# Kernel optimization log

Hardware: AMD Instinct MI355X
Metric: run time of the kernel (lower is better)

## Reference

```python
import jax, jax.numpy as jnp
import numpy as np

B, S, D = 4, 2048, 256


def setup_inputs() -> dict:
    key = jax.random.key(0)
    ks = jax.random.split(key, 8)
    context = jax.random.normal(ks[0], (B, S, D), dtype=jnp.float32)
    eos_mask = jax.random.randint(ks[1], (B, S, S), 0, 2, dtype=jnp.int32)
    prior = jax.random.uniform(ks[2], (B, S, S), dtype=jnp.float32)
    Wq = jax.random.normal(ks[3], (D, D), dtype=jnp.float32) * 0.02
    bq = jnp.zeros((D,), dtype=jnp.float32)
    Wk = jax.random.normal(ks[4], (D, D), dtype=jnp.float32) * 0.02
    bk = jnp.zeros((D,), dtype=jnp.float32)
    ln_a = jnp.ones((D,), dtype=jnp.float32)
    ln_b = jnp.zeros((D,), dtype=jnp.float32)
    return {"context": context, "prior": prior, "Wq": Wq, "bq": bq,
            "Wk": Wk, "bk": bk, "ln_a": ln_a, "ln_b": ln_b,
            "eos_mask": eos_mask}


def reference(context, prior, Wq, bq, Wk, bk, ln_a, ln_b, eos_mask):
    seq = context.shape[1]
    # LayerNorm (torch: unbiased std, eps added to std)
    mean = context.mean(axis=-1, keepdims=True)
    std = jnp.std(context, axis=-1, ddof=1, keepdims=True)
    x = ln_a * (context - mean) / (std + 1e-6) + ln_b

    idx = jnp.arange(seq)
    diff = idx[None, :] - idx[:, None]
    a = diff == 1                      # superdiagonal
    offdiag = jnp.abs(diff) == 1       # a + c (super + sub diagonal)
    eye = diff == 0                    # b
    tri = jnp.triu(jnp.ones((seq, seq), dtype=jnp.float32))

    # mask = eos_mask & (a + c)  (precedence: & binds looser than +)
    mask = jnp.bitwise_and(eos_mask, offdiag.astype(jnp.int32))

    # torch Linear: y = x @ W.T + b
    query = x @ Wq.T + bq
    key = x @ Wk.T + bk
    scores = jnp.einsum('bqd,bkd->bqk', query, key) / 256.0
    scores = jnp.where(mask == 0, -1e9, scores)
    neibor = jax.nn.softmax(scores, axis=-1)
    neibor = jnp.sqrt(neibor * neibor.transpose(0, 2, 1) + 1e-9)
    neibor = prior + (1.0 - prior) * neibor

    # log -> zero except superdiagonal -> triangular matmul -> exp
    t = jnp.where(a, jnp.log(neibor + 1e-9), 0.0) @ tri   # [B,S,S]
    g = jnp.exp(jnp.matmul(tri, t))                        # [B,S,S]
    strict_upper = jnp.logical_and(tri.astype(bool), jnp.logical_not(eye))
    g = jnp.where(strict_upper, g, 0.0)  # masked_fill(tri - b == 0, 0)
    g = g + g.transpose(0, 2, 1) + jnp.where(eye, neibor, 1e-9)
    return g
```

## Files before the change

### kernel.cpp

```cpp
#include <hip/hip_runtime.h>
#include <math.h>

#define SS 2048
#define DD 256
#define NB 4
#define NR (NB * SS)

__global__ __launch_bounds__(256) void prep_kernel(
    const float* __restrict__ Wq, const float* __restrict__ Wk,
    const float* __restrict__ bq, float* __restrict__ A, float* __restrict__ u) {
    int t = threadIdx.x;
    int d = blockIdx.x;
    if (d < DD) {
        float a0 = 0.f, a1 = 0.f, a2 = 0.f, a3 = 0.f;
        for (int i = 0; i < DD; i += 4) {
            a0 += Wq[(i + 0) * DD + d] * Wk[(i + 0) * DD + t];
            a1 += Wq[(i + 1) * DD + d] * Wk[(i + 1) * DD + t];
            a2 += Wq[(i + 2) * DD + d] * Wk[(i + 2) * DD + t];
            a3 += Wq[(i + 3) * DD + d] * Wk[(i + 3) * DD + t];
        }
        A[d * DD + t] = (a0 + a1) + (a2 + a3);
    } else {
        float a0 = 0.f, a1 = 0.f, a2 = 0.f, a3 = 0.f;
        for (int i = 0; i < DD; i += 4) {
            a0 += Wk[(i + 0) * DD + t] * bq[i + 0];
            a1 += Wk[(i + 1) * DD + t] * bq[i + 1];
            a2 += Wk[(i + 2) * DD + t] * bq[i + 2];
            a3 += Wk[(i + 3) * DD + t] * bq[i + 3];
        }
        u[t] = (a0 + a1) + (a2 + a3);
    }
}

#define XP 260
#define FMA4(accv, a, bv) \
    accv.x += (a) * bv.x; accv.y += (a) * bv.y; \
    accv.z += (a) * bv.z; accv.w += (a) * bv.w;

__global__ __launch_bounds__(256) void gemm_score_kernel(
    const float4* __restrict__ ctx4, const float4* __restrict__ ln_a4,
    const float4* __restrict__ ln_b4, const float* __restrict__ A,
    const float* __restrict__ u, const int* __restrict__ eos,
    float4* __restrict__ pvals) {
    __shared__ float Xn[34][XP];
    int tid = threadIdx.x;
    int lane = tid & 63;
    int wave = tid >> 6;
    int row0 = blockIdx.x * 32;
    const float4* A4 = (const float4*)A;

    float4 ga = ln_a4[lane], gb = ln_b4[lane];
    for (int rr = wave; rr < 34; rr += 4) {
        int g = row0 - 1 + rr;
        g = (g < 0) ? 0 : (g > NR - 1 ? NR - 1 : g);
        float4 v = ctx4[(size_t)g * 64 + lane];
        float s = v.x + v.y + v.z + v.w;
#pragma unroll
        for (int off = 32; off > 0; off >>= 1) s += __shfl_xor(s, off, 64);
        float mean = s * (1.0f / 256.0f);
        float4 dd = make_float4(v.x - mean, v.y - mean, v.z - mean, v.w - mean);
        float s2 = dd.x * dd.x + dd.y * dd.y + dd.z * dd.z + dd.w * dd.w;
#pragma unroll
        for (int off = 32; off > 0; off >>= 1) s2 += __shfl_xor(s2, off, 64);
        float inv = 1.0f / (sqrtf(s2 * (1.0f / 255.0f)) + 1e-6f);
        float* xr = &Xn[rr][lane * 4];
        xr[0] = ga.x * dd.x * inv + gb.x;
        xr[1] = ga.y * dd.y * inv + gb.y;
        xr[2] = ga.z * dd.z * inv + gb.z;
        xr[3] = ga.w * dd.w * inv + gb.w;
    }
    __syncthreads();

    int tx = tid & 15, ty = tid >> 4;
    float4 acc[2][4] = {};
    const float* xr0 = &Xn[1 + ty * 2][0];
    const float* xr1 = &Xn[2 + ty * 2][0];
#pragma unroll 4
    for (int k = 0; k < DD; k++) {
        float a0 = xr0[k];
        float a1 = xr1[k];
        float4 b0 = A4[(size_t)k * 64 + tx];
        float4 b1 = A4[(size_t)k * 64 + tx + 16];
        float4 b2 = A4[(size_t)k * 64 + tx + 32];
        float4 b3 = A4[(size_t)k * 64 + tx + 48];
        FMA4(acc[0][0], a0, b0) FMA4(acc[0][1], a0, b1)
        FMA4(acc[0][2], a0, b2) FMA4(acc[0][3], a0, b3)
        FMA4(acc[1][0], a1, b0) FMA4(acc[1][1], a1, b1)
        FMA4(acc[1][2], a1, b2) FMA4(acc[1][3], a1, b3)
    }

    const float4* u4 = (const float4*)u;
#pragma unroll
    for (int q = 0; q < 4; q++) {
        float4 uv = u4[q * 16 + tx];
        acc[0][q].x += uv.x; acc[0][q].y += uv.y; acc[0][q].z += uv.z; acc[0][q].w += uv.w;
        acc[1][q].x += uv.x; acc[1][q].y += uv.y; acc[1][q].z += uv.z; acc[1][q].w += uv.w;
    }
#pragma unroll
    for (int i = 0; i < 2; i++) {
        int li = 1 + ty * 2 + i;
        int r = row0 + ty * 2 + i;
        int s = r & (SS - 1), b = r >> 11;
        bool has_n = (s < SS - 1), has_p = (s > 0);
        float fn = has_n ? 1.0f : 0.0f, fp = has_p ? 1.0f : 0.0f;
        float partial = 0.0f;
#pragma unroll
        for (int q = 0; q < 4; q++) {
            int c = q * 64 + tx * 4;
            float wx = fn * Xn[li + 1][c + 0] - fp * Xn[li - 1][c + 0];
            float wy = fn * Xn[li + 1][c + 1] - fp * Xn[li - 1][c + 1];
            float wz = fn * Xn[li + 1][c + 2] - fp * Xn[li - 1][c + 2];
            float ww = fn * Xn[li + 1][c + 3] - fp * Xn[li - 1][c + 3];
            partial += acc[i][q].x * wx + acc[i][q].y * wy
                     + acc[i][q].z * wz + acc[i][q].w * ww;
        }
#pragma unroll
        for (int off = 8; off > 0; off >>= 1) partial += __shfl_xor(partial, off, 64);
        if (tx == 0) {
            size_t base = (size_t)b * SS * SS + (size_t)s * SS;
            bool mn = has_n && (eos[base + s + 1] != 0);
            bool mp = has_p && (eos[base + s - 1] != 0);
            float pn, pp, pd;
            if (mn && mp) {
                float d = partial * (1.0f / 256.0f);
                pn = 1.0f / (1.0f + __expf(-d));
                pp = 1.0f - pn;
                pd = 0.0f;
            } else if (mn) { pn = 1.0f; pp = 0.0f; pd = 0.0f; }
            else if (mp)   { pn = 0.0f; pp = 1.0f; pd = 0.0f; }
            else           { pn = pp = pd = (1.0f / 2048.0f); }
            pvals[r] = make_float4(pn, pp, pd, 0.0f);
        }
    }
}

__global__ __launch_bounds__(256) void scan_kernel(
    const float4* __restrict__ pvals, const float* __restrict__ prior,
    float* __restrict__ P) {
    int b = blockIdx.x, t = threadIdx.x;
    int base_s = t * 8;
    double loc[8];
    double run = 0.0;
#pragma unroll
    for (int i = 0; i < 8; i++) {
        loc[i] = run;
        int s = base_s + i;
        float lv = 0.0f;
        if (s < SS - 1) {
            int r = b * SS + s;
            float4 pv = pvals[r];
            float4 pv1 = pvals[r + 1];
            float ns = sqrtf(pv.x * pv1.y + 1e-9f);
            float pr = prior[(size_t)b * SS * SS + (size_t)s * SS + s + 1];
            float neib = pr + (1.0f - pr) * ns;
            lv = logf(neib + 1e-9f);
        }
        run += (double)lv;
    }
    int lane = t & 63, wave = t >> 6;
    double v = run;
#pragma unroll
    for (int off = 1; off < 64; off <<= 1) {
        double uu = __shfl_up(v, off, 64);
        if (lane >= off) v += uu;
    }
    __shared__ double wsum[4];
    if (lane == 63) wsum[wave] = v;
    __syncthreads();
    double woff = 0.0;
    for (int w = 0; w < wave; w++) woff += wsum[w];
    double texcl = woff + (v - run);
#pragma unroll
    for (int i = 0; i < 8; i++)
        P[b * SS + base_s + i] = (float)(texcl + loc[i]);
}

__global__ __launch_bounds__(256) void fill_kernel(
    const float* __restrict__ P, const float4* __restrict__ pvals,
    const float* __restrict__ prior, float* __restrict__ out) {
    int blk = blockIdx.x;
    int i = blk & (SS - 1), b = blk >> 11;
    int t = threadIdx.x;
    __shared__ float shPi, shDv;
    if (t == 0) {
        shPi = P[blk];
        float pd = pvals[blk].z;
        float prd = prior[(size_t)b * SS * SS + (size_t)i * SS + i];
        shDv = prd + (1.0f - prd) * sqrtf(pd * pd + 1e-9f);
    }
    __syncthreads();
    float Pi = shPi, dv = shDv;
    const float* Pb = P + b * SS;
    size_t outbase = (size_t)blk * SS;
    float4 pj0 = *(const float4*)(Pb + t * 8);
    float4 pj1 = *(const float4*)(Pb + t * 8 + 4);
    float pj[8] = {pj0.x, pj0.y, pj0.z, pj0.w, pj1.x, pj1.y, pj1.z, pj1.w};
    float res[8];
#pragma unroll
    for (int k = 0; k < 8; k++) {
        int j = t * 8 + k;
        float d = (j > i) ? (pj[k] - Pi) : (Pi - pj[k]);
        float val = __expf(d) + 1e-9f;
        res[k] = (j == i) ? dv : val;
    }
    *(float4*)(out + outbase + t * 8) = make_float4(res[0], res[1], res[2], res[3]);
    *(float4*)(out + outbase + t * 8 + 4) = make_float4(res[4], res[5], res[6], res[7]);
}

extern "C" void kernel_launch(void* const* d_in, const int* in_sizes, int n_in,
                              void* d_out, int out_size, void* d_ws, size_t ws_size,
                              hipStream_t stream) {
    const float* context = (const float*)d_in[0];
    const float* prior   = (const float*)d_in[1];
    const float* Wq      = (const float*)d_in[2];
    const float* bq      = (const float*)d_in[3];
    const float* Wk      = (const float*)d_in[4];
    const float* ln_a    = (const float*)d_in[6];
    const float* ln_b    = (const float*)d_in[7];
    const int*   eos     = (const int*)d_in[8];
    float* out = (float*)d_out;

    float* ws = (float*)d_ws;
    float* A     = ws;
    float* u     = ws + 65536;
    float4* pv   = (float4*)(ws + 65792);
    float* P     = ws + 98560;

    prep_kernel<<<DD + 1, 256, 0, stream>>>(Wq, Wk, bq, A, u);
    gemm_score_kernel<<<NR / 32, 256, 0, stream>>>(
        (const float4*)context, (const float4*)ln_a, (const float4*)ln_b,
        A, u, eos, pv);
    scan_kernel<<<NB, 256, 0, stream>>>(pv, prior, P);
    fill_kernel<<<NR, 256, 0, stream>>>(P, pv, prior, out);
}
```

Before: 250.4 us.

## Stage A tiles in LDS and use a transposed X tile in the score GEMM

The score GEMM is restructured. Each block now stages 32x256 chunks of A in shared memory and keeps a transposed copy of the normalized rows, so each thread computes a 4-row by 8-column tile with float4 LDS reads instead of streaming A from global memory per thread. Partial dot products are reduced across waves through a small shared buffer. This raises LDS use to roughly 104 KB per block, which lowers occupancy and adds barriers, to cut global traffic on A. The whole output still comes from the fill kernel, which likely dominates the run time.

```diff
diff --git a/kernel.cpp b/kernel.cpp
--- a/kernel.cpp
+++ b/kernel.cpp
@@ -33,6 +33,7 @@
 }
 
 #define XP 260
+#define XTP 36
 #define FMA4(accv, a, bv) \
     accv.x += (a) * bv.x; accv.y += (a) * bv.y; \
     accv.z += (a) * bv.z; accv.w += (a) * bv.w;
@@ -43,6 +44,9 @@
     const float* __restrict__ u, const int* __restrict__ eos,
     float4* __restrict__ pvals) {
     __shared__ float Xn[34][XP];
+    __shared__ float XnT[256][XTP];
+    __shared__ float As[32][256];
+    __shared__ float red[32][4];
     int tid = threadIdx.x;
     int lane = tid & 63;
     int wave = tid >> 6;
@@ -71,66 +75,99 @@
     }
     __syncthreads();
 
-    int tx = tid & 15, ty = tid >> 4;
-    float4 acc[2][4] = {};
-    const float* xr0 = &Xn[1 + ty * 2][0];
-    const float* xr1 = &Xn[2 + ty * 2][0];
-#pragma unroll 4
-    for (int k = 0; k < DD; k++) {
-        float a0 = xr0[k];
-        float a1 = xr1[k];
-        float4 b0 = A4[(size_t)k * 64 + tx];
-        float4 b1 = A4[(size_t)k * 64 + tx + 16];
-        float4 b2 = A4[(size_t)k * 64 + tx + 32];
-        float4 b3 = A4[(size_t)k * 64 + tx + 48];
-        FMA4(acc[0][0], a0, b0) FMA4(acc[0][1], a0, b1)
-        FMA4(acc[0][2], a0, b2) FMA4(acc[0][3], a0, b3)
-        FMA4(acc[1][0], a1, b0) FMA4(acc[1][1], a1, b1)
-        FMA4(acc[1][2], a1, b2) FMA4(acc[1][3], a1, b3)
+    {
+        int r = tid >> 3;
+        int kq = (tid & 7) * 32;
+        const float* src = &Xn[1 + r][kq];
+#pragma unroll
+        for (int j = 0; j < 32; j++) XnT[kq + j][r] = src[j];
+    }
+
+    int lx = lane & 7;
+    int ly = lane >> 3;
+    float4 acc[4][2] = {};
+    const float4* As4 = (const float4*)As;
+    int bidx = wave * 16 + lx * 2;
+    for (int k0 = 0; k0 < DD; k0 += 32) {
+#pragma unroll
+        for (int q = 0; q < 8; q++) {
+            int f4 = q * 256 + tid;
+            int k = f4 >> 6, c4 = f4 & 63;
+            *(float4*)&As[k][c4 * 4] = A4[(size_t)(k0 + k) * 64 + c4];
+        }
+        __syncthreads();
+        const float4* pX = (const float4*)&XnT[k0][0] + ly;
+        const float4* pB = As4 + bidx;
+#pragma unroll 8
+        for (int k = 0; k < 32; k++) {
+            float4 a4 = pX[k * 9];
+            float4 b0 = pB[k * 64];
+            float4 b1 = pB[k * 64 + 1];
+            FMA4(acc[0][0], a4.x, b0) FMA4(acc[0][1], a4.x, b1)
+            FMA4(acc[1][0], a4.y, b0) FMA4(acc[1][1], a4.y, b1)
+            FMA4(acc[2][0], a4.z, b0) FMA4(acc[2][1], a4.z, b1)
+            FMA4(acc[3][0], a4.w, b0) FMA4(acc[3][1], a4.w, b1)
+        }
+        __syncthreads();
     }
 
     const float4* u4 = (const float4*)u;
-#pragma unroll
-    for (int q = 0; q < 4; q++) {
-        float4 uv = u4[q * 16 + tx];
-        acc[0][q].x += uv.x; acc[0][q].y += uv.y; acc[0][q].z += uv.z; acc[0][q].w += uv.w;
-        acc[1][q].x += uv.x; acc[1][q].y += uv.y; acc[1][q].z += uv.z; acc[1][q].w += uv.w;
-    }
-#pragma unroll
-    for (int i = 0; i < 2; i++) {
-        int li = 1 + ty * 2 + i;
-        int r = row0 + ty * 2 + i;
+    {
+        float4 uv0 = u4[bidx], uv1 = u4[bidx + 1];
+#pragma unroll
+        for (int i = 0; i < 4; i++) {
+            acc[i][0].x += uv0.x; acc[i][0].y += uv0.y;
+            acc[i][0].z += uv0.z; acc[i][0].w += uv0.w;
+            acc[i][1].x += uv1.x; acc[i][1].y += uv1.y;
+            acc[i][1].z += uv1.z; acc[i][1].w += uv1.w;
+        }
+    }
+    int c = wave * 64 + lx * 8;
+#pragma unroll
+    for (int i = 0; i < 4; i++) {
+        int row = ly * 4 + i;
+        int li = 1 + row;
+        int r = row0 + row;
+        int s = r & (SS - 1);
+        bool has_n = (s < SS - 1), has_p = (s > 0);
+        float fn = has_n ? 1.0f : 0.0f, fp = has_p ? 1.0f : 0.0f;
+        float4 n0 = *(const float4*)&Xn[li + 1][c];
+        float4 n1 = *(const float4*)&Xn[li + 1][c + 4];
+        float4 p0 = *(const float4*)&Xn[li - 1][c];
+        float4 p1 = *(const float4*)&Xn[li - 1][c + 4];
+        float partial =
+            acc[i][0].x * (fn * n0.x - fp * p0.x) +
+            acc[i][0].y * (fn * n0.y - fp * p0.y) +
+            acc[i][0].z * (fn * n0.z - fp * p0.z) +
+            acc[i][0].w * (fn * n0.w - fp * p0.w) +
+            acc[i][1].x * (fn * n1.x - fp * p1.x) +
+            acc[i][1].y * (fn * n1.y - fp * p1.y) +
+            acc[i][1].z * (fn * n1.z - fp * p1.z) +
+            acc[i][1].w * (fn * n1.w - fp * p1.w);
+#pragma unroll
+        for (int off = 4; off > 0; off >>= 1) partial += __shfl_xor(partial, off, 64);
+        if (lx == 0) red[row][wave] = partial;
+    }
+    __syncthreads();
+    if (tid < 32) {
+        int row = tid;
+        int r = row0 + row;
         int s = r & (SS - 1), b = r >> 11;
         bool has_n = (s < SS - 1), has_p = (s > 0);
-        float fn = has_n ? 1.0f : 0.0f, fp = has_p ? 1.0f : 0.0f;
-        float partial = 0.0f;
-#pragma unroll
-        for (int q = 0; q < 4; q++) {
-            int c = q * 64 + tx * 4;
-            float wx = fn * Xn[li + 1][c + 0] - fp * Xn[li - 1][c + 0];
-            float wy = fn * Xn[li + 1][c + 1] - fp * Xn[li - 1][c + 1];
-            float wz = fn * Xn[li + 1][c + 2] - fp * Xn[li - 1][c + 2];
-            float ww = fn * Xn[li + 1][c + 3] - fp * Xn[li - 1][c + 3];
-            partial += acc[i][q].x * wx + acc[i][q].y * wy
-                     + acc[i][q].z * wz + acc[i][q].w * ww;
-        }
-#pragma unroll
-        for (int off = 8; off > 0; off >>= 1) partial += __shfl_xor(partial, off, 64);
-        if (tx == 0) {
-            size_t base = (size_t)b * SS * SS + (size_t)s * SS;
-            bool mn = has_n && (eos[base + s + 1] != 0);
-            bool mp = has_p && (eos[base + s - 1] != 0);
-            float pn, pp, pd;
-            if (mn && mp) {
-                float d = partial * (1.0f / 256.0f);
-                pn = 1.0f / (1.0f + __expf(-d));
-                pp = 1.0f - pn;
-                pd = 0.0f;
-            } else if (mn) { pn = 1.0f; pp = 0.0f; pd = 0.0f; }
-            else if (mp)   { pn = 0.0f; pp = 1.0f; pd = 0.0f; }
-            else           { pn = pp = pd = (1.0f / 2048.0f); }
-            pvals[r] = make_float4(pn, pp, pd, 0.0f);
-        }
+        float partial = (red[row][0] + red[row][1]) + (red[row][2] + red[row][3]);
+        size_t base = (size_t)b * SS * SS + (size_t)s * SS;
+        bool mn = has_n && (eos[base + s + 1] != 0);
+        bool mp = has_p && (eos[base + s - 1] != 0);
+        float pn, pp, pd;
+        if (mn && mp) {
+            float d = partial * (1.0f / 256.0f);
+            pn = 1.0f / (1.0f + __expf(-d));
+            pp = 1.0f - pn;
+            pd = 0.0f;
+        } else if (mn) { pn = 1.0f; pp = 0.0f; pd = 0.0f; }
+        else if (mp)   { pn = 0.0f; pp = 1.0f; pd = 0.0f; }
+        else           { pn = pp = pd = (1.0f / 2048.0f); }
+        pvals[r] = make_float4(pn, pp, pd, 0.0f);
     }
 }
 
```

New measurement: 227.7 us. 9.0% less time.

## Stage projection matrix tiles in LDS and give each wave eight rows

Applied to the files above, without the earlier changes.

The score GEMM now loads 64-row tiles of the combined Wq^T·Wk matrix into shared memory. Each wave computes eight normalized rows against all 256 output columns, reusing every LDS value across eight rows. This replaces the per-thread global reads of A, which were repeated for every row pair. The cost is a large LDS footprint (about 99KB per block), extra barriers, and a different reduction that collects per-row dot products by wave-wide shuffles.

```diff
diff --git a/kernel.cpp b/kernel.cpp
--- a/kernel.cpp
+++ b/kernel.cpp
@@ -33,6 +33,7 @@
 }
 
 #define XP 260
+#define BK 64
 #define FMA4(accv, a, bv) \
     accv.x += (a) * bv.x; accv.y += (a) * bv.y; \
     accv.z += (a) * bv.z; accv.w += (a) * bv.w;
@@ -43,6 +44,7 @@
     const float* __restrict__ u, const int* __restrict__ eos,
     float4* __restrict__ pvals) {
     __shared__ float Xn[34][XP];
+    __shared__ float As[BK][256];
     int tid = threadIdx.x;
     int lane = tid & 63;
     int wave = tid >> 6;
@@ -63,74 +65,101 @@
 #pragma unroll
         for (int off = 32; off > 0; off >>= 1) s2 += __shfl_xor(s2, off, 64);
         float inv = 1.0f / (sqrtf(s2 * (1.0f / 255.0f)) + 1e-6f);
-        float* xr = &Xn[rr][lane * 4];
-        xr[0] = ga.x * dd.x * inv + gb.x;
-        xr[1] = ga.y * dd.y * inv + gb.y;
-        xr[2] = ga.z * dd.z * inv + gb.z;
-        xr[3] = ga.w * dd.w * inv + gb.w;
-    }
-    __syncthreads();
-
-    int tx = tid & 15, ty = tid >> 4;
-    float4 acc[2][4] = {};
-    const float* xr0 = &Xn[1 + ty * 2][0];
-    const float* xr1 = &Xn[2 + ty * 2][0];
+        float4 xv;
+        xv.x = ga.x * dd.x * inv + gb.x;
+        xv.y = ga.y * dd.y * inv + gb.y;
+        xv.z = ga.z * dd.z * inv + gb.z;
+        xv.w = ga.w * dd.w * inv + gb.w;
+        *(float4*)&Xn[rr][lane * 4] = xv;
+    }
+
+    float4 acc[8] = {};
+    const float4* As4 = (const float4*)As;
+    int rbase = 1 + wave * 8;
+    for (int k0 = 0; k0 < DD; k0 += BK) {
+        __syncthreads();
+#pragma unroll
+        for (int q = 0; q < (BK * 64) / 256; q++) {
+            int f4 = q * 256 + tid;
+            int k = f4 >> 6, c4 = f4 & 63;
+            *(float4*)&As[k][c4 * 4] = A4[(size_t)(k0 + k) * 64 + c4];
+        }
+        __syncthreads();
 #pragma unroll 4
-    for (int k = 0; k < DD; k++) {
-        float a0 = xr0[k];
-        float a1 = xr1[k];
-        float4 b0 = A4[(size_t)k * 64 + tx];
-        float4 b1 = A4[(size_t)k * 64 + tx + 16];
-        float4 b2 = A4[(size_t)k * 64 + tx + 32];
-        float4 b3 = A4[(size_t)k * 64 + tx + 48];
-        FMA4(acc[0][0], a0, b0) FMA4(acc[0][1], a0, b1)
-        FMA4(acc[0][2], a0, b2) FMA4(acc[0][3], a0, b3)
-        FMA4(acc[1][0], a1, b0) FMA4(acc[1][1], a1, b1)
-        FMA4(acc[1][2], a1, b2) FMA4(acc[1][3], a1, b3)
-    }
-
-    const float4* u4 = (const float4*)u;
-#pragma unroll
-    for (int q = 0; q < 4; q++) {
-        float4 uv = u4[q * 16 + tx];
-        acc[0][q].x += uv.x; acc[0][q].y += uv.y; acc[0][q].z += uv.z; acc[0][q].w += uv.w;
-        acc[1][q].x += uv.x; acc[1][q].y += uv.y; acc[1][q].z += uv.z; acc[1][q].w += uv.w;
-    }
-#pragma unroll
-    for (int i = 0; i < 2; i++) {
-        int li = 1 + ty * 2 + i;
-        int r = row0 + ty * 2 + i;
+        for (int kk = 0; kk < BK; kk += 4) {
+            float4 av[8];
+#pragma unroll
+            for (int i = 0; i < 8; i++)
+                av[i] = *(const float4*)&Xn[rbase + i][k0 + kk];
+            float4 b;
+            b = As4[(size_t)(kk + 0) * 64 + lane];
+            FMA4(acc[0], av[0].x, b) FMA4(acc[1], av[1].x, b)
+            FMA4(acc[2], av[2].x, b) FMA4(acc[3], av[3].x, b)
+            FMA4(acc[4], av[4].x, b) FMA4(acc[5], av[5].x, b)
+            FMA4(acc[6], av[6].x, b) FMA4(acc[7], av[7].x, b)
+            b = As4[(size_t)(kk + 1) * 64 + lane];
+            FMA4(acc[0], av[0].y, b) FMA4(acc[1], av[1].y, b)
+            FMA4(acc[2], av[2].y, b) FMA4(acc[3], av[3].y, b)
+            FMA4(acc[4], av[4].y, b) FMA4(acc[5], av[5].y, b)
+            FMA4(acc[6], av[6].y, b) FMA4(acc[7], av[7].y, b)
+            b = As4[(size_t)(kk + 2) * 64 + lane];
+            FMA4(acc[0], av[0].z, b) FMA4(acc[1], av[1].z, b)
+            FMA4(acc[2], av[2].z, b) FMA4(acc[3], av[3].z, b)
+            FMA4(acc[4], av[4].z, b) FMA4(acc[5], av[5].z, b)
+            FMA4(acc[6], av[6].z, b) FMA4(acc[7], av[7].z, b)
+            b = As4[(size_t)(kk + 3) * 64 + lane];
+            FMA4(acc[0], av[0].w, b) FMA4(acc[1], av[1].w, b)
+            FMA4(acc[2], av[2].w, b) FMA4(acc[3], av[3].w, b)
+            FMA4(acc[4], av[4].w, b) FMA4(acc[5], av[5].w, b)
+            FMA4(acc[6], av[6].w, b) FMA4(acc[7], av[7].w, b)
+        }
+    }
+
+    {
+        float4 uv = ((const float4*)u)[lane];
+#pragma unroll
+        for (int i = 0; i < 8; i++) {
+            acc[i].x += uv.x; acc[i].y += uv.y;
+            acc[i].z += uv.z; acc[i].w += uv.w;
+        }
+    }
+    float myp = 0.0f;
+#pragma unroll
+    for (int i = 0; i < 8; i++) {
+        int li = rbase + i;
+        int r = row0 + wave * 8 + i;
+        int s = r & (SS - 1);
+        float fn = (s < SS - 1) ? 1.0f : 0.0f;
+        float fp = (s > 0) ? 1.0f : 0.0f;
+        float4 n1 = *(const float4*)&Xn[li + 1][lane * 4];
+        float4 p1 = *(const float4*)&Xn[li - 1][lane * 4];
+        float partial =
+            acc[i].x * (fn * n1.x - fp * p1.x) +
+            acc[i].y * (fn * n1.y - fp * p1.y) +
+            acc[i].z * (fn * n1.z - fp * p1.z) +
+            acc[i].w * (fn * n1.w - fp * p1.w);
+#pragma unroll
+        for (int off = 32; off > 0; off >>= 1)
+            partial += __shfl_xor(partial, off, 64);
+        myp = (lane == i) ? partial : myp;
+    }
+    if (lane < 8) {
+        int r = row0 + wave * 8 + lane;
         int s = r & (SS - 1), b = r >> 11;
         bool has_n = (s < SS - 1), has_p = (s > 0);
-        float fn = has_n ? 1.0f : 0.0f, fp = has_p ? 1.0f : 0.0f;
-        float partial = 0.0f;
-#pragma unroll
-        for (int q = 0; q < 4; q++) {
-            int c = q * 64 + tx * 4;
-            float wx = fn * Xn[li + 1][c + 0] - fp * Xn[li - 1][c + 0];
-            float wy = fn * Xn[li + 1][c + 1] - fp * Xn[li - 1][c + 1];
-            float wz = fn * Xn[li + 1][c + 2] - fp * Xn[li - 1][c + 2];
-            float ww = fn * Xn[li + 1][c + 3] - fp * Xn[li - 1][c + 3];
-            partial += acc[i][q].x * wx + acc[i][q].y * wy
-                     + acc[i][q].z * wz + acc[i][q].w * ww;
-        }
-#pragma unroll
-        for (int off = 8; off > 0; off >>= 1) partial += __shfl_xor(partial, off, 64);
-        if (tx == 0) {
-            size_t base = (size_t)b * SS * SS + (size_t)s * SS;
-            bool mn = has_n && (eos[base + s + 1] != 0);
-            bool mp = has_p && (eos[base + s - 1] != 0);
-            float pn, pp, pd;
-            if (mn && mp) {
-                float d = partial * (1.0f / 256.0f);
-                pn = 1.0f / (1.0f + __expf(-d));
-                pp = 1.0f - pn;
-                pd = 0.0f;
-            } else if (mn) { pn = 1.0f; pp = 0.0f; pd = 0.0f; }
-            else if (mp)   { pn = 0.0f; pp = 1.0f; pd = 0.0f; }
-            else           { pn = pp = pd = (1.0f / 2048.0f); }
-            pvals[r] = make_float4(pn, pp, pd, 0.0f);
-        }
+        size_t base = (size_t)b * SS * SS + (size_t)s * SS;
+        bool mn = has_n && (eos[base + s + 1] != 0);
+        bool mp = has_p && (eos[base + s - 1] != 0);
+        float pn, pp, pd;
+        if (mn && mp) {
+            float d = myp * (1.0f / 256.0f);
+            pn = 1.0f / (1.0f + __expf(-d));
+            pp = 1.0f - pn;
+            pd = 0.0f;
+        } else if (mn) { pn = 1.0f; pp = 0.0f; pd = 0.0f; }
+        else if (mp)   { pn = 0.0f; pp = 1.0f; pd = 0.0f; }
+        else           { pn = pp = pd = (1.0f / 2048.0f); }
+        pvals[r] = make_float4(pn, pp, pd, 0.0f);
     }
 }
 
```

Measured after the change: 225.4 us. -10.0%, faster.

## Stage A matrix tiles in shared memory with register double-buffering

Applied to the files above, without the earlier changes.

The GEMM loop in the score kernel now copies 64-row chunks of the 256x256 A matrix into LDS cooperatively, instead of having every thread read A straight from global memory each k step. The inner loop is software-pipelined: the LDS operands for step k+2 are loaded while the FMAs for step k run. This targets global/L2 load latency in a loop bound by memory reads. In exchange it adds 64 KB of LDS per block, which can cut occupancy, plus one barrier per chunk.

```diff
diff --git a/kernel.cpp b/kernel.cpp
--- a/kernel.cpp
+++ b/kernel.cpp
@@ -32,6 +32,7 @@
     }
 }
 
+#define BK 64
 #define XP 260
 #define FMA4(accv, a, bv) \
     accv.x += (a) * bv.x; accv.y += (a) * bv.y; \
@@ -43,6 +44,7 @@
     const float* __restrict__ u, const int* __restrict__ eos,
     float4* __restrict__ pvals) {
     __shared__ float Xn[34][XP];
+    __shared__ float As[BK][256];
     int tid = threadIdx.x;
     int lane = tid & 63;
     int wave = tid >> 6;
@@ -69,24 +71,46 @@
         xr[2] = ga.z * dd.z * inv + gb.z;
         xr[3] = ga.w * dd.w * inv + gb.w;
     }
-    __syncthreads();
 
     int tx = tid & 15, ty = tid >> 4;
     float4 acc[2][4] = {};
     const float* xr0 = &Xn[1 + ty * 2][0];
     const float* xr1 = &Xn[2 + ty * 2][0];
+
+#define LOADK(kk, s) \
+    a0##s = xr0[k0 + (kk)]; a1##s = xr1[k0 + (kk)]; \
+    b0##s = *(const float4*)&As[(kk)][tx * 4]; \
+    b1##s = *(const float4*)&As[(kk)][tx * 4 + 64]; \
+    b2##s = *(const float4*)&As[(kk)][tx * 4 + 128]; \
+    b3##s = *(const float4*)&As[(kk)][tx * 4 + 192];
+#define DOFMA(s) \
+    FMA4(acc[0][0], a0##s, b0##s) FMA4(acc[0][1], a0##s, b1##s) \
+    FMA4(acc[0][2], a0##s, b2##s) FMA4(acc[0][3], a0##s, b3##s) \
+    FMA4(acc[1][0], a1##s, b0##s) FMA4(acc[1][1], a1##s, b1##s) \
+    FMA4(acc[1][2], a1##s, b2##s) FMA4(acc[1][3], a1##s, b3##s)
+
+    for (int k0 = 0; k0 < DD; k0 += BK) {
+        __syncthreads();
+#pragma unroll
+        for (int q = 0; q < (BK * 64) / 256; q++) {
+            int f4 = q * 256 + tid;
+            int k = f4 >> 6, c4 = f4 & 63;
+            *(float4*)&As[k][c4 * 4] = A4[(size_t)(k0 + k) * 64 + c4];
+        }
+        __syncthreads();
+        float a0A, a1A, a0B, a1B;
+        float4 b0A, b1A, b2A, b3A, b0B, b1B, b2B, b3B;
+        LOADK(0, A)
+        LOADK(1, B)
 #pragma unroll 4
-    for (int k = 0; k < DD; k++) {
-        float a0 = xr0[k];
-        float a1 = xr1[k];
-        float4 b0 = A4[(size_t)k * 64 + tx];
-        float4 b1 = A4[(size_t)k * 64 + tx + 16];
-        float4 b2 = A4[(size_t)k * 64 + tx + 32];
-        float4 b3 = A4[(size_t)k * 64 + tx + 48];
-        FMA4(acc[0][0], a0, b0) FMA4(acc[0][1], a0, b1)
-        FMA4(acc[0][2], a0, b2) FMA4(acc[0][3], a0, b3)
-        FMA4(acc[1][0], a1, b0) FMA4(acc[1][1], a1, b1)
-        FMA4(acc[1][2], a1, b2) FMA4(acc[1][3], a1, b3)
+        for (int k = 0; k < BK - 2; k += 2) {
+            DOFMA(A)
+            LOADK(k + 2, A)
+            DOFMA(B)
+            LOADK(k + 3, B)
+        }
+        DOFMA(A)
+        DOFMA(B)
     }
 
     const float4* u4 = (const float4*)u;
```

After: 230.0 us. -8.2%, faster.
